# Kernel tuning notes

Measured on AMD Instinct MI355X. Metric: run time of the kernel, lower is better.

The kernel has to match this reference:

```python
import jax, jax.numpy as jnp
import numpy as np


def setup_inputs() -> dict:
    key = jax.random.key(0)
    k1, k2, k3, k4 = jax.random.split(key, 4)
    B, I, O, N, T = 4096, 512, 64, 32, 4
    E = N * T
    x = jax.random.normal(k1, (B, I), dtype=jnp.float32)
    dst_state = jax.random.uniform(k2, (B, N), dtype=jnp.float32)
    type_state = jax.random.uniform(k3, (B, T), dtype=jnp.float32)
    # orthogonal init with gain=0.01 approximated by small random weights; bias=0
    W = jax.random.normal(k4, (E, I, O), dtype=jnp.float32) * 0.01
    b = jnp.zeros((E, O), dtype=jnp.float32)
    return {"x": x, "dst_state": dst_state, "type_state": type_state, "W": W, "b": b}


def reference(x, dst_state, type_state, W, b):
    # gating weights: outer product of dst_state [B,N] and type_state [B,T],
    # flattened to [B, E] with E = N*T (row-major, matching torch view)
    B = x.shape[0]
    g = (dst_state[:, :, None] * type_state[:, None, :]).reshape(B, -1)  # [B,E]
    # per-expert linear then gated sum over experts, fused via einsum
    logits = jnp.einsum("bi,eio,be->bo", x, W, g) + jnp.einsum("be,eo->bo", g, b)
    # torch.distributions.Categorical(logits=...) normalizes logits
    return jax.nn.log_softmax(logits, axis=-1)
```

## Files before the change

### kernel.cpp

```cpp
#include <hip/hip_runtime.h>
#include <hip/hip_bf16.h>

typedef __bf16 bf16x8 __attribute__((ext_vector_type(8)));
typedef float  f32x4  __attribute__((ext_vector_type(4)));

#define B_SZ 4096
#define I_SZ 512
#define O_SZ 64
#define E_SZ 128
#define BM   256
#define G_EXP 8
#define EG_N  16
#define MT_N  16

__global__ void prep_x(const float* __restrict__ x, __bf16* __restrict__ xb) {
  int i = blockIdx.x * 256 + threadIdx.x;
  float4 v = ((const float4*)x)[i];
  union { __bf16 h[4]; ushort4 u4; } pk;
  pk.h[0] = (__bf16)v.x; pk.h[1] = (__bf16)v.y;
  pk.h[2] = (__bf16)v.z; pk.h[3] = (__bf16)v.w;
  ((ushort4*)xb)[i] = pk.u4;
}

__global__ void prep_w(const float* __restrict__ W, __bf16* __restrict__ wt) {
  __shared__ __bf16 tile[64][66];
  int e  = blockIdx.x >> 3;
  int it = blockIdx.x & 7;
  const float* src = W + (size_t)e * I_SZ * O_SZ + (size_t)it * 64 * O_SZ;
  #pragma unroll
  for (int s = 0; s < 16; ++s) {
    int idx = s * 256 + threadIdx.x;
    int r = idx >> 6, o = idx & 63;
    tile[o][r] = (__bf16)src[idx];
  }
  __syncthreads();
  __bf16* dst = wt + (size_t)e * O_SZ * I_SZ + it * 64;
  #pragma unroll
  for (int s = 0; s < 4; ++s) {
    int idx = s * 256 + threadIdx.x;
    int o = idx >> 4, c = (idx & 15) << 2;
    union { __bf16 h[4]; ushort4 u4; } q;
    q.h[0] = tile[o][c + 0]; q.h[1] = tile[o][c + 1];
    q.h[2] = tile[o][c + 2]; q.h[3] = tile[o][c + 3];
    *(ushort4*)&dst[(size_t)o * I_SZ + c] = q.u4;
  }
}

__global__ void prep_g(const float* __restrict__ ds, const float* __restrict__ ts,
                       float* __restrict__ gT) {
  int idx = blockIdx.x * 256 + threadIdx.x;
  int e = idx >> 12, b = idx & 4095;
  gT[idx] = ds[b * 32 + (e >> 2)] * ts[b * 4 + (e & 3)];
}

__global__ __launch_bounds__(512, 2)
void mtc_gemm(const __bf16* __restrict__ xb, const __bf16* __restrict__ wt,
              const float* __restrict__ gT, float* __restrict__ partials) {
  __shared__ __align__(16) __bf16 wsh[2][O_SZ * I_SZ];
  __shared__ float gsh[G_EXP][BM];

  const int tid  = threadIdx.x;
  const int wave = tid >> 6;
  const int lane = tid & 63;

  int bid = (int)blockIdx.x;
  bid = (bid & 7) * 32 + (bid >> 3);
  const int mtile = bid & 15;
  const int eg    = bid >> 4;
  const int row0  = mtile * BM;
  const int e0    = eg * G_EXP;

  for (int idx = tid; idx < G_EXP * BM; idx += 512)
    gsh[idx >> 8][idx & 255] =
        gT[(size_t)(e0 + (idx >> 8)) * B_SZ + row0 + (idx & 255)];

  bf16x8 af[2][16];
  {
    const __bf16* xr = xb + (size_t)(row0 + wave * 32 + (lane & 15)) * I_SZ
                          + (lane >> 4) * 8;
    #pragma unroll
    for (int mf = 0; mf < 2; ++mf)
      #pragma unroll
      for (int j = 0; j < 16; ++j)
        af[mf][j] = *(const bf16x8*)(xr + mf * 16 * I_SZ + j * 32);
  }

  auto stage = [&](int sbuf, int e) {
    const __bf16* wsrc = wt + (size_t)(e0 + e) * O_SZ * I_SZ;
    #pragma unroll
    for (int i = 0; i < 8; ++i) {
      int o = i * 8 + wave;
      int q = lane ^ (o & 7);
      __builtin_amdgcn_global_load_lds(
          (const __attribute__((address_space(1))) void*)(wsrc + (size_t)o * I_SZ + q * 8),
          (__attribute__((address_space(3))) void*)(&wsh[sbuf][o * I_SZ]),
          16, 0, 0);
    }
  };

  __syncthreads();

  stage(0, 0);

  f32x4 logits[2][4] = {};

  int buf = 0;
  for (int e = 0; e < G_EXP; ++e) {
    if (e < G_EXP - 1) {
      stage(buf ^ 1, e + 1);
      asm volatile("s_waitcnt vmcnt(8)" ::: "memory");
    } else {
      asm volatile("s_waitcnt vmcnt(0)" ::: "memory");
    }
    __builtin_amdgcn_s_barrier();

    f32x4 acc[2][4] = {};
    const __bf16* wb = &wsh[buf][0];
    __builtin_amdgcn_s_setprio(1);
    #pragma unroll
    for (int j = 0; j < 16; ++j) {
      bf16x8 bfr[4];
      #pragma unroll
      for (int nf = 0; nf < 4; ++nf) {
        int o  = nf * 16 + (lane & 15);
        int q  = j * 4 + (lane >> 4);
        int ph = q ^ (o & 7);
        bfr[nf] = *(const bf16x8*)(wb + (size_t)o * I_SZ + ph * 8);
      }
      #pragma unroll
      for (int nf = 0; nf < 4; ++nf)
        #pragma unroll
        for (int mf = 0; mf < 2; ++mf)
          acc[mf][nf] = __builtin_amdgcn_mfma_f32_16x16x32_bf16(
              af[mf][j], bfr[nf], acc[mf][nf], 0, 0, 0);
    }
    __builtin_amdgcn_s_setprio(0);

    f32x4 gq[2];
    #pragma unroll
    for (int mf = 0; mf < 2; ++mf)
      gq[mf] = *(const f32x4*)&gsh[e][wave * 32 + mf * 16 + (lane >> 4) * 4];
    #pragma unroll
    for (int mf = 0; mf < 2; ++mf)
      #pragma unroll
      for (int nf = 0; nf < 4; ++nf)
        #pragma unroll
        for (int rg = 0; rg < 4; ++rg)
          logits[mf][nf][rg] += gq[mf][rg] * acc[mf][nf][rg];

    __builtin_amdgcn_s_barrier();
    buf ^= 1;
  }

  float* pout = partials + (size_t)eg * B_SZ * O_SZ + (size_t)row0 * O_SZ;
  #pragma unroll
  for (int mf = 0; mf < 2; ++mf)
    #pragma unroll
    for (int nf = 0; nf < 4; ++nf)
      #pragma unroll
      for (int rg = 0; rg < 4; ++rg) {
        int r = wave * 32 + mf * 16 + ((lane >> 4) << 2) + rg;
        int o = nf * 16 + (lane & 15);
        pout[(size_t)r * O_SZ + o] = logits[mf][nf][rg];
      }
}

__global__ __launch_bounds__(256)
void mtc_reduce(const float* __restrict__ partials, const float* __restrict__ gT,
                const float* __restrict__ bias, float* __restrict__ out) {
  __shared__ float bsh[E_SZ * O_SZ];
  for (int i = threadIdx.x; i < E_SZ * O_SZ; i += 256) bsh[i] = bias[i];
  __syncthreads();
  int wave = threadIdx.x >> 6, lane = threadIdx.x & 63;
  int r = blockIdx.x * 4 + wave;
  float s = 0.f;
  #pragma unroll
  for (int k = 0; k < EG_N; ++k)
    s += partials[(size_t)k * B_SZ * O_SZ + (size_t)r * O_SZ + lane];
  float bacc = 0.f;
  for (int e = 0; e < E_SZ; ++e)
    bacc += gT[(size_t)e * B_SZ + r] * bsh[e * O_SZ + lane];
  s += bacc;
  float m = s;
  #pragma unroll
  for (int off = 32; off; off >>= 1) m = fmaxf(m, __shfl_xor(m, off));
  float ex = expf(s - m), sum = ex;
  #pragma unroll
  for (int off = 32; off; off >>= 1) sum += __shfl_xor(sum, off);
  out[(size_t)r * O_SZ + lane] = s - m - logf(sum);
}

extern "C" void kernel_launch(void* const* d_in, const int* in_sizes, int n_in,
                              void* d_out, int out_size, void* d_ws, size_t ws_size,
                              hipStream_t stream) {
  const float* x    = (const float*)d_in[0];
  const float* ds   = (const float*)d_in[1];
  const float* ts   = (const float*)d_in[2];
  const float* W    = (const float*)d_in[3];
  const float* bias = (const float*)d_in[4];
  float* out = (float*)d_out;

  char* w = (char*)d_ws;
  __bf16* xb      = (__bf16*)(w);
  __bf16* wt      = (__bf16*)(w + (4ull  << 20));
  float*  gT      = (float*) (w + (12ull << 20));
  float*  parts   = (float*) (w + (14ull << 20));

  prep_x    <<<2048, 256, 0, stream>>>(x, xb);
  prep_w    <<<1024, 256, 0, stream>>>(W, wt);
  prep_g    <<<2048, 256, 0, stream>>>(ds, ts, gT);
  mtc_gemm  <<< 256, 512, 0, stream>>>(xb, wt, gT, parts);
  mtc_reduce<<<1024, 256, 0, stream>>>(parts, gT, bias, out);
}
```

Baseline: 66.71 us.

## Fuse gate prep into x prep, fold bias into GEMM, split weight staging

Merges the gate-product computation into the x-to-bf16 conversion kernel, which removes one launch. The bias term moves into the GEMM by initialising each expert's accumulators with that expert's bias before gating, so the reduce kernel no longer loops over 128 experts per row. The weight prefetch for the next expert is split into four chunks interleaved with the MFMA sub-loops, with a barrier after each chunk, and the first stage is issued before the x and gate loads. The extra barriers per expert could add synchronisation cost.

```diff
diff --git a/kernel.cpp b/kernel.cpp
--- a/kernel.cpp
+++ b/kernel.cpp
@@ -13,13 +13,17 @@
 #define EG_N  16
 #define MT_N  16
 
-__global__ void prep_x(const float* __restrict__ x, __bf16* __restrict__ xb) {
+__global__ void prep_xg(const float* __restrict__ x, __bf16* __restrict__ xb,
+                        const float* __restrict__ ds, const float* __restrict__ ts,
+                        float* __restrict__ gT) {
   int i = blockIdx.x * 256 + threadIdx.x;
   float4 v = ((const float4*)x)[i];
   union { __bf16 h[4]; ushort4 u4; } pk;
   pk.h[0] = (__bf16)v.x; pk.h[1] = (__bf16)v.y;
   pk.h[2] = (__bf16)v.z; pk.h[3] = (__bf16)v.w;
   ((ushort4*)xb)[i] = pk.u4;
+  int e = i >> 12, b = i & 4095;
+  gT[i] = ds[b * 32 + (e >> 2)] * ts[b * 4 + (e & 3)];
 }
 
 __global__ void prep_w(const float* __restrict__ W, __bf16* __restrict__ wt) {
@@ -46,16 +50,10 @@
   }
 }
 
-__global__ void prep_g(const float* __restrict__ ds, const float* __restrict__ ts,
-                       float* __restrict__ gT) {
-  int idx = blockIdx.x * 256 + threadIdx.x;
-  int e = idx >> 12, b = idx & 4095;
-  gT[idx] = ds[b * 32 + (e >> 2)] * ts[b * 4 + (e & 3)];
-}
-
 __global__ __launch_bounds__(512, 2)
 void mtc_gemm(const __bf16* __restrict__ xb, const __bf16* __restrict__ wt,
-              const float* __restrict__ gT, float* __restrict__ partials) {
+              const float* __restrict__ gT, const float* __restrict__ bias,
+              float* __restrict__ partials) {
   __shared__ __align__(16) __bf16 wsh[2][O_SZ * I_SZ];
   __shared__ float gsh[G_EXP][BM];
 
@@ -70,26 +68,11 @@
   const int row0  = mtile * BM;
   const int e0    = eg * G_EXP;
 
-  for (int idx = tid; idx < G_EXP * BM; idx += 512)
-    gsh[idx >> 8][idx & 255] =
-        gT[(size_t)(e0 + (idx >> 8)) * B_SZ + row0 + (idx & 255)];
-
-  bf16x8 af[2][16];
-  {
-    const __bf16* xr = xb + (size_t)(row0 + wave * 32 + (lane & 15)) * I_SZ
-                          + (lane >> 4) * 8;
-    #pragma unroll
-    for (int mf = 0; mf < 2; ++mf)
-      #pragma unroll
-      for (int j = 0; j < 16; ++j)
-        af[mf][j] = *(const bf16x8*)(xr + mf * 16 * I_SZ + j * 32);
-  }
-
-  auto stage = [&](int sbuf, int e) {
+  auto stage2 = [&](int sbuf, int e, int s) {
     const __bf16* wsrc = wt + (size_t)(e0 + e) * O_SZ * I_SZ;
     #pragma unroll
-    for (int i = 0; i < 8; ++i) {
-      int o = i * 8 + wave;
+    for (int ii = 0; ii < 2; ++ii) {
+      int o = (s * 2 + ii) * 8 + wave;
       int q = lane ^ (o & 7);
       __builtin_amdgcn_global_load_lds(
           (const __attribute__((address_space(1))) void*)(wsrc + (size_t)o * I_SZ + q * 8),
@@ -98,43 +81,66 @@
     }
   };
 
+  #pragma unroll
+  for (int s = 0; s < 4; ++s) stage2(0, 0, s);
+
+  for (int idx = tid; idx < G_EXP * BM; idx += 512)
+    gsh[idx >> 8][idx & 255] =
+        gT[(size_t)(e0 + (idx >> 8)) * B_SZ + row0 + (idx & 255)];
+
+  bf16x8 af[2][16];
+  {
+    const __bf16* xr = xb + (size_t)(row0 + wave * 32 + (lane & 15)) * I_SZ
+                          + (lane >> 4) * 8;
+    #pragma unroll
+    for (int mf = 0; mf < 2; ++mf)
+      #pragma unroll
+      for (int j = 0; j < 16; ++j)
+        af[mf][j] = *(const bf16x8*)(xr + mf * 16 * I_SZ + j * 32);
+  }
+
   __syncthreads();
 
-  stage(0, 0);
-
   f32x4 logits[2][4] = {};
-
   int buf = 0;
   for (int e = 0; e < G_EXP; ++e) {
-    if (e < G_EXP - 1) {
-      stage(buf ^ 1, e + 1);
-      asm volatile("s_waitcnt vmcnt(8)" ::: "memory");
-    } else {
-      asm volatile("s_waitcnt vmcnt(0)" ::: "memory");
+    float bv[4];
+    #pragma unroll
+    for (int nf = 0; nf < 4; ++nf)
+      bv[nf] = bias[(size_t)(e0 + e) * O_SZ + nf * 16 + (lane & 15)];
+    f32x4 acc[2][4];
+    #pragma unroll
+    for (int mf = 0; mf < 2; ++mf)
+      #pragma unroll
+      for (int nf = 0; nf < 4; ++nf)
+        acc[mf][nf] = (f32x4){bv[nf], bv[nf], bv[nf], bv[nf]};
+
+    const __bf16* wb = &wsh[buf][0];
+    #pragma unroll
+    for (int s = 0; s < 4; ++s) {
+      if (e < G_EXP - 1) stage2(buf ^ 1, e + 1, s);
+      __builtin_amdgcn_s_setprio(1);
+      #pragma unroll
+      for (int jj = 0; jj < 4; ++jj) {
+        const int j = s * 4 + jj;
+        bf16x8 bfr[4];
+        #pragma unroll
+        for (int nf = 0; nf < 4; ++nf) {
+          int o  = nf * 16 + (lane & 15);
+          int q  = j * 4 + (lane >> 4);
+          int ph = q ^ (o & 7);
+          bfr[nf] = *(const bf16x8*)(wb + (size_t)o * I_SZ + ph * 8);
+        }
+        #pragma unroll
+        for (int nf = 0; nf < 4; ++nf)
+          #pragma unroll
+          for (int mf = 0; mf < 2; ++mf)
+            acc[mf][nf] = __builtin_amdgcn_mfma_f32_16x16x32_bf16(
+                af[mf][j], bfr[nf], acc[mf][nf], 0, 0, 0);
+      }
+      __builtin_amdgcn_s_setprio(0);
+      __builtin_amdgcn_s_barrier();
     }
-    __builtin_amdgcn_s_barrier();
-
-    f32x4 acc[2][4] = {};
-    const __bf16* wb = &wsh[buf][0];
-    __builtin_amdgcn_s_setprio(1);
-    #pragma unroll
-    for (int j = 0; j < 16; ++j) {
-      bf16x8 bfr[4];
-      #pragma unroll
-      for (int nf = 0; nf < 4; ++nf) {
-        int o  = nf * 16 + (lane & 15);
-        int q  = j * 4 + (lane >> 4);
-        int ph = q ^ (o & 7);
-        bfr[nf] = *(const bf16x8*)(wb + (size_t)o * I_SZ + ph * 8);
-      }
-      #pragma unroll
-      for (int nf = 0; nf < 4; ++nf)
-        #pragma unroll
-        for (int mf = 0; mf < 2; ++mf)
-          acc[mf][nf] = __builtin_amdgcn_mfma_f32_16x16x32_bf16(
-              af[mf][j], bfr[nf], acc[mf][nf], 0, 0, 0);
-    }
-    __builtin_amdgcn_s_setprio(0);
 
     f32x4 gq[2];
     #pragma unroll
@@ -148,6 +154,7 @@
         for (int rg = 0; rg < 4; ++rg)
           logits[mf][nf][rg] += gq[mf][rg] * acc[mf][nf][rg];
 
+    asm volatile("s_waitcnt vmcnt(0)" ::: "memory");
     __builtin_amdgcn_s_barrier();
     buf ^= 1;
   }
@@ -166,21 +173,13 @@
 }
 
 __global__ __launch_bounds__(256)
-void mtc_reduce(const float* __restrict__ partials, const float* __restrict__ gT,
-                const float* __restrict__ bias, float* __restrict__ out) {
-  __shared__ float bsh[E_SZ * O_SZ];
-  for (int i = threadIdx.x; i < E_SZ * O_SZ; i += 256) bsh[i] = bias[i];
-  __syncthreads();
+void mtc_reduce(const float* __restrict__ partials, float* __restrict__ out) {
   int wave = threadIdx.x >> 6, lane = threadIdx.x & 63;
   int r = blockIdx.x * 4 + wave;
   float s = 0.f;
   #pragma unroll
   for (int k = 0; k < EG_N; ++k)
     s += partials[(size_t)k * B_SZ * O_SZ + (size_t)r * O_SZ + lane];
-  float bacc = 0.f;
-  for (int e = 0; e < E_SZ; ++e)
-    bacc += gT[(size_t)e * B_SZ + r] * bsh[e * O_SZ + lane];
-  s += bacc;
   float m = s;
   #pragma unroll
   for (int off = 32; off; off >>= 1) m = fmaxf(m, __shfl_xor(m, off));
@@ -206,9 +205,8 @@
   float*  gT      = (float*) (w + (12ull << 20));
   float*  parts   = (float*) (w + (14ull << 20));
 
-  prep_x    <<<2048, 256, 0, stream>>>(x, xb);
+  prep_xg   <<<2048, 256, 0, stream>>>(x, xb, ds, ts, gT);
   prep_w    <<<1024, 256, 0, stream>>>(W, wt);
-  prep_g    <<<2048, 256, 0, stream>>>(ds, ts, gT);
-  mtc_gemm  <<< 256, 512, 0, stream>>>(xb, wt, gT, parts);
-  mtc_reduce<<<1024, 256, 0, stream>>>(parts, gT, bias, out);
-}
+  mtc_gemm  <<< 256, 512, 0, stream>>>(xb, wt, gT, bias, parts);
+  mtc_reduce<<<1024, 256, 0, stream>>>(parts, out);
+}
```

Result: faster. 63.53 us (-4.8%).
